# Optimization experiments

Measured on AMD Instinct MI355X. Metric: run time of the kernel, lower is better.

## Reference

```python
import jax, jax.numpy as jnp
import numpy as np


def _bce_logits(x, t):
    # numerically stable BCEWithLogits (pos_weight=1), elementwise
    return jnp.maximum(x, 0.0) - x * t + jnp.log1p(jnp.exp(-jnp.abs(x)))


def _ciou(box1, box2, eps=1e-9):
    # box1, box2: [n,4] in (cx, cy, w, h); matches bbox_iou(..., x1y1x2y2=False, CIoU=True)
    b1x1, b1x2 = box1[:, 0] - box1[:, 2] / 2, box1[:, 0] + box1[:, 2] / 2
    b1y1, b1y2 = box1[:, 1] - box1[:, 3] / 2, box1[:, 1] + box1[:, 3] / 2
    b2x1, b2x2 = box2[:, 0] - box2[:, 2] / 2, box2[:, 0] + box2[:, 2] / 2
    b2y1, b2y2 = box2[:, 1] - box2[:, 3] / 2, box2[:, 1] + box2[:, 3] / 2
    inter = (jnp.clip(jnp.minimum(b1x2, b2x2) - jnp.maximum(b1x1, b2x1), 0.0)
             * jnp.clip(jnp.minimum(b1y2, b2y2) - jnp.maximum(b1y1, b2y1), 0.0))
    w1, h1 = b1x2 - b1x1, b1y2 - b1y1 + eps
    w2, h2 = b2x2 - b2x1, b2y2 - b2y1 + eps
    union = w1 * h1 + w2 * h2 - inter + eps
    iou = inter / union
    cw = jnp.maximum(b1x2, b2x2) - jnp.minimum(b1x1, b2x1)
    ch = jnp.maximum(b1y2, b2y2) - jnp.minimum(b1y1, b2y1)
    c2 = cw ** 2 + ch ** 2 + eps
    rho2 = ((b2x1 + b2x2 - b1x1 - b1x2) ** 2 + (b2y1 + b2y2 - b1y1 - b1y2) ** 2) / 4.0
    v = (4.0 / jnp.pi ** 2) * (jnp.arctan(w2 / h2) - jnp.arctan(w1 / h1)) ** 2
    alpha = jax.lax.stop_gradient(v / (1.0 + eps - iou + v))  # torch.no_grad()
    return iou - (rho2 / c2 + v * alpha)


def _layer_loss(preds, targets, anchors, li):
    # preds: [B, na, H, W, 5+nc]; targets: [nt,6]; anchors: [n_layers, na, 2]
    B, na, H, W, C = preds.shape
    nt = targets.shape[0]
    ai = jnp.arange(na, dtype=preds.dtype)
    # targets.repeat(na,1,1) with anchor index appended -> [na, nt, 7]
    t7 = jnp.concatenate([jnp.broadcast_to(targets[None], (na, nt, 6)),
                          jnp.broadcast_to(ai[:, None, None], (na, nt, 1))], axis=2)
    gain = jnp.array([1.0, 1.0, W, H, W, H, 1.0], dtype=preds.dtype)
    t = t7 * gain
    # anchor-ratio filter: max(r, 1/r).max(-1) < 4 (as boolean mask instead of fancy-index)
    r = t[:, :, 4:6] / anchors[li][:, None, :]                  # [na, nt, 2]
    mask = jnp.max(jnp.maximum(r, 1.0 / r), axis=2) < 4.0       # [na, nt]
    tf = t.reshape(na * nt, 7)
    m = mask.reshape(-1)
    mf = m.astype(preds.dtype)
    b = tf[:, 0].astype(jnp.int32)
    c = tf[:, 1].astype(jnp.int32)
    gxy = tf[:, 2:4]
    gwh = tf[:, 4:6]
    gij = gxy.astype(jnp.int32)  # .long() truncation (coords >= 0)
    gi = jnp.clip(gij[:, 0], 0, W - 1)
    gj = jnp.clip(gij[:, 1], 0, H - 1)
    a = tf[:, 6].astype(jnp.int32)
    # faithful to original: anch = anchors[a] then forward takes [range(n), a] => anchors[a, a]
    anch = anchors[a, a]
    # img_ids = unique(batch ids).flip(); with full 0..B-1 coverage lookup == B-1-b
    match = (B - 1) - b
    ps = preds[match, a, gj, gi]                                # [na*nt, C] gather
    pxy = jax.nn.sigmoid(ps[:, :2])
    pwh = jnp.exp(ps[:, 2:4]) * anch
    pbox = jnp.concatenate([pxy, pwh], axis=1)
    tbox = jnp.concatenate([gxy - gij.astype(gxy.dtype), gwh], axis=1)
    iou = _ciou(pbox, tbox)
    nvalid = jnp.maximum(mf.sum(), 1.0)
    lbox = ((1.0 - iou) * mf).sum() / nvalid                    # mean over matched targets
    # scatter detached clamped iou into tobj; invalid rows get OOB batch idx -> dropped
    scatter_b = jnp.where(m, match, B)
    tobj = jnp.zeros((B, na, H, W), preds.dtype).at[scatter_b, a, gj, gi].set(
        jax.lax.stop_gradient(jnp.clip(iou, 0.0)) * mf)
    nc = C - 5
    t1h = jax.nn.one_hot(c, nc, dtype=preds.dtype)
    lcls = (_bce_logits(ps[:, 5:], t1h) * mf[:, None]).sum() / (nvalid * nc)
    lobj = _bce_logits(preds[..., 4], tobj).mean()
    return lbox, lobj, lcls


def setup_inputs() -> dict:
    key = jax.random.key(0)
    ks = jax.random.split(key, 6)
    p0 = jax.random.normal(ks[0], (16, 3, 80, 80, 85), jnp.float32)
    p1 = jax.random.normal(ks[1], (16, 3, 40, 40, 85), jnp.float32)
    p2 = jax.random.normal(ks[2], (16, 3, 20, 20, 85), jnp.float32)
    nt, B = 300, 16
    img = (jnp.arange(nt) % B).astype(jnp.float32)  # every batch id present
    cls = jax.random.randint(ks[3], (nt,), 0, 80).astype(jnp.float32)
    xy = jax.random.uniform(ks[4], (nt, 2), minval=0.05, maxval=0.95)
    wh = jax.random.uniform(ks[5], (nt, 2), minval=0.02, maxval=0.2)
    targets = jnp.concatenate([img[:, None], cls[:, None], xy, wh], axis=1)
    anchors = jnp.array([[[1.25, 1.625], [2.0, 3.75], [4.125, 2.875]],
                         [[1.875, 3.8125], [3.875, 2.8125], [3.6875, 7.4375]],
                         [[3.625, 2.8125], [4.875, 6.1875], [11.65625, 10.1875]]],
                        dtype=jnp.float32)
    return {"p0": p0, "p1": p1, "p2": p2, "targets": targets, "anchors": anchors}


def reference(p0, p1, p2, targets, anchors):
    lb = lo = lc = 0.0
    for li, p in enumerate((p0, p1, p2)):
        a_, b_, c_ = _layer_loss(p, targets, anchors, li)
        lb = lb + a_
        lo = lo + b_
        lc = lc + c_
    lbox = lb * 0.05
    lobj = lo * 1.0
    lcls = lc * 0.5
    loss = lbox + lobj + lcls
    stats = jnp.stack([lbox, lobj, lcls, loss])
    return (jnp.reshape(loss, (1,)), stats)
```

## Files before the change

kernel.cpp:

```cpp
#include <hip/hip_runtime.h>
#include <math.h>

#define NT    300
#define NA    3
#define BATCH 16
#define NCLS  80
#define CCH   85
#define NROWS 2700
#define NBO   394
#define NBT   675
#define NBLK  (NBO + NBT)
#define HASHSZ 4096


__device__ __forceinline__ float softplusf(float x) {
    return fmaxf(x, 0.f) + log1pf(expf(-fabsf(x)));
}

__device__ __forceinline__ double block_reduce(double v, double* red) {
    #pragma unroll
    for (int off = 32; off > 0; off >>= 1) v += __shfl_down(v, off, 64);
    const int wid = threadIdx.x >> 6, lane = threadIdx.x & 63;
    if (lane == 0) red[wid] = v;
    __syncthreads();
    double r = (threadIdx.x < 4) ? red[threadIdx.x] : 0.0;
    r += __shfl_down(r, 2, 64);
    r += __shfl_down(r, 1, 64);
    __syncthreads();
    return r;
}

__global__ __launch_bounds__(256) void main_kernel(
    const float* __restrict__ p0, const float* __restrict__ p1,
    const float* __restrict__ p2,
    const float* __restrict__ targets, const float* __restrict__ anchors,
    char* __restrict__ ws)
{
    __shared__ double red[4];

    double* obj_part = (double*)(ws);
    float*  row_lbox = (float*)(ws + 3200);
    float*  row_lcls = (float*)(ws + 14000);
    float*  row_nval = (float*)(ws + 24800);
    int*    row_key  = (int*)(ws + 35600);
    float*  row_val  = (float*)(ws + 46400);

    if (blockIdx.x < NBO) {
        const int ob = blockIdx.x;
        int li, bb;
        if (ob < 300)      { li = 0; bb = ob; }
        else if (ob < 375) { li = 1; bb = ob - 300; }
        else               { li = 2; bb = ob - 375; }
        const float* p = (li == 0) ? p0 : ((li == 1) ? p1 : p2);
        const int N = (BATCH * NA * 6400) >> (2*li);

        float s = 0.f;
        #pragma unroll
        for (int k = 0; k < 4; ++k) {
            const int idx = bb * 1024 + k * 256 + threadIdx.x;
            if (idx < N) s += softplusf(p[(size_t)idx * CCH + 4]);
        }
        const double t = block_reduce((double)s, red);
        if (threadIdx.x == 0) obj_part[ob] = t;
        return;
    }

    const int gr   = (blockIdx.x - NBO) * 4 + (threadIdx.x >> 6);
    const int lane = threadIdx.x & 63;
    const int li   = gr / (NA * NT);
    const int r    = gr - li * (NA * NT);
    const int a    = r / NT;
    const int ti   = r - a * NT;
    const float* p = (li == 0) ? p0 : ((li == 1) ? p1 : p2);
    const int W = 80 >> li, H = W;

    const float img = targets[ti*6 + 0];
    const float cls = targets[ti*6 + 1];
    const float tx  = targets[ti*6 + 2] * (float)W;
    const float ty  = targets[ti*6 + 3] * (float)H;
    const float tw  = targets[ti*6 + 4] * (float)W;
    const float th  = targets[ti*6 + 5] * (float)H;

    const float ax = anchors[(li*3 + a)*2 + 0];
    const float ay = anchors[(li*3 + a)*2 + 1];
    const float rx = tw / ax, ry = th / ay;
    const float mr = fmaxf(fmaxf(rx, 1.f/rx), fmaxf(ry, 1.f/ry));
    const bool  mask = mr < 4.f;
    const float mf = mask ? 1.f : 0.f;

    const int b = (int)img;
    const int c = (int)cls;
    const int gij_x = (int)tx;
    const int gij_y = (int)ty;
    const int gi = min(max(gij_x, 0), W - 1);
    const int gj = min(max(gij_y, 0), H - 1);

    const float anch_x = anchors[(a*3 + a)*2 + 0];
    const float anch_y = anchors[(a*3 + a)*2 + 1];

    const int match = BATCH - 1 - b;
    const int cell  = ((match*NA + a)*H + gj)*W + gi;
    const float* ps = p + (size_t)cell * CCH;

    const float x1 = ps[lane];
    const float x2 = (lane < CCH - 64) ? ps[64 + lane] : 0.f;

    const float s0   = __shfl(x1, 0);
    const float s1   = __shfl(x1, 1);
    const float s2   = __shfl(x1, 2);
    const float s3   = __shfl(x1, 3);
    const float objx = __shfl(x1, 4);

    const int ch = 5 + c;
    float contrib = (lane >= 5) ? softplusf(x1) : 0.f;
    if (lane < CCH - 64) contrib += softplusf(x2);
    if (lane == ch) contrib -= x1;
    if (ch >= 64 && lane == ch - 64) contrib -= x2;
    #pragma unroll
    for (int off = 32; off > 0; off >>= 1)
        contrib += __shfl_down(contrib, off, 64);

    const float pxx = 1.f / (1.f + expf(-s0));
    const float pyy = 1.f / (1.f + expf(-s1));
    const float pw  = expf(s2) * anch_x;
    const float ph  = expf(s3) * anch_y;
    const float fx  = tx - (float)gij_x;
    const float fy  = ty - (float)gij_y;

    const float eps = 1e-9f;
    const float b1x1 = pxx - pw*0.5f, b1x2 = pxx + pw*0.5f;
    const float b1y1 = pyy - ph*0.5f, b1y2 = pyy + ph*0.5f;
    const float b2x1 = fx - tw*0.5f,  b2x2 = fx + tw*0.5f;
    const float b2y1 = fy - th*0.5f,  b2y2 = fy + th*0.5f;
    float iw = fminf(b1x2, b2x2) - fmaxf(b1x1, b2x1); iw = fmaxf(iw, 0.f);
    float ih = fminf(b1y2, b2y2) - fmaxf(b1y1, b2y1); ih = fmaxf(ih, 0.f);
    const float inter = iw * ih;
    const float w1 = b1x2 - b1x1, h1 = b1y2 - b1y1 + eps;
    const float w2 = b2x2 - b2x1, h2 = b2y2 - b2y1 + eps;
    const float uni = w1*h1 + w2*h2 - inter + eps;
    const float iou = inter / uni;
    const float cw  = fmaxf(b1x2, b2x2) - fminf(b1x1, b2x1);
    const float chh = fmaxf(b1y2, b2y2) - fminf(b1y1, b2y1);
    const float c2 = cw*cw + chh*chh + eps;
    const float dx = b2x1 + b2x2 - b1x1 - b1x2;
    const float dy = b2y1 + b2y2 - b1y1 - b1y2;
    const float rho2 = (dx*dx + dy*dy) * 0.25f;
    const float dat = atanf(w2/h2) - atanf(w1/h1);
    const float v = 0.40528473456935108577f * dat * dat;
    const float alpha = v / (1.f + eps - iou + v);
    const float ciou = iou - (rho2/c2 + v*alpha);

    if (lane == 0) {
        row_lbox[gr] = (1.f - ciou) * mf;
        row_lcls[gr] = contrib * mf;
        row_nval[gr] = mf;
        row_key[gr]  = mask ? ((li << 20) | cell) : -1;
        row_val[gr]  = mask ? objx * fmaxf(ciou, 0.f) : 0.f;
    }
}

__global__ __launch_bounds__(256) void final_kernel(
    const char* __restrict__ ws, float* __restrict__ out)
{
    __shared__ double red[4];
    __shared__ int hkey[HASHSZ];
    __shared__ int hrow[HASHSZ];

    const double* obj_part = (const double*)(ws);
    const float*  row_lbox = (const float*)(ws + 3200);
    const float*  row_lcls = (const float*)(ws + 14000);
    const float*  row_nval = (const float*)(ws + 24800);
    const int*    row_key  = (const int*)(ws + 35600);
    const float*  row_val  = (const float*)(ws + 46400);

    for (int q = threadIdx.x; q < HASHSZ; q += 256) { hkey[q] = -1; hrow[q] = -1; }
    __syncthreads();

    double so[3] = {0, 0, 0};
    for (int bk = threadIdx.x; bk < NBO; bk += 256) {
        const double v = obj_part[bk];
        if (bk < 300)      so[0] += v;
        else if (bk < 375) so[1] += v;
        else               so[2] += v;
    }

    int    slots[11];
    int    nm = 0;
    double lb[3] = {0,0,0}, lc[3] = {0,0,0}, nv[3] = {0,0,0}, co[3] = {0,0,0};

    for (int i = threadIdx.x; i < NROWS; i += 256) {
        const int l = i / (NA * NT);
        lb[l] += (double)row_lbox[i];
        lc[l] += (double)row_lcls[i];
        nv[l] += (double)row_nval[i];
        const int k = row_key[i];
        int s = -1;
        if (k >= 0) {
            unsigned h = ((unsigned)k * 2654435761u) >> 20;
            s = (int)(h & (HASHSZ - 1));
            while (true) {
                const int prev = atomicCAS(&hkey[s], -1, k);
                if (prev == -1 || prev == k) { atomicMax(&hrow[s], i); break; }
                s = (s + 1) & (HASHSZ - 1);
            }
        }
        slots[nm++] = s;
    }
    __syncthreads();
    nm = 0;
    for (int i = threadIdx.x; i < NROWS; i += 256) {
        const int s = slots[nm++];
        if (s >= 0 && hrow[s] == i)
            co[i / (NA * NT)] += (double)row_val[i];
    }

    double rsum[12];
    #pragma unroll
    for (int l = 0; l < 3; ++l) {
        rsum[l*4 + 0] = block_reduce(lb[l], red);
        rsum[l*4 + 1] = block_reduce(lc[l], red);
        rsum[l*4 + 2] = block_reduce(co[l], red);
        rsum[l*4 + 3] = block_reduce(nv[l], red);
        so[l]         = block_reduce(so[l], red);
    }

    if (threadIdx.x == 0) {
        double lbox = 0.0, lobj = 0.0, lcls = 0.0;
        for (int l = 0; l < 3; ++l) {
            const double nvv = fmax(rsum[l*4 + 3], 1.0);
            lbox += rsum[l*4 + 0] / nvv;
            lcls += rsum[l*4 + 1] / (nvv * (double)NCLS);
            const double N = (double)((BATCH * NA * 6400) >> (2*l));
            lobj += (so[l] - rsum[l*4 + 2]) / N;
        }
        lbox *= 0.05;
        lcls *= 0.5;
        const double loss = lbox + lobj + lcls;
        out[0] = (float)loss;
        out[1] = (float)lbox;
        out[2] = (float)lobj;
        out[3] = (float)lcls;
        out[4] = (float)loss;
    }
}

extern "C" void kernel_launch(void* const* d_in, const int* in_sizes, int n_in,
                              void* d_out, int out_size, void* d_ws, size_t ws_size,
                              hipStream_t stream) {
    const float* p0      = (const float*)d_in[0];
    const float* p1      = (const float*)d_in[1];
    const float* p2      = (const float*)d_in[2];
    const float* targets = (const float*)d_in[3];
    const float* anchors = (const float*)d_in[4];

    main_kernel<<<NBLK, 256, 0, stream>>>(p0, p1, p2, targets, anchors,
                                          (char*)d_ws);
    final_kernel<<<1, 256, 0, stream>>>((const char*)d_ws, (float*)d_out);
}
```

Measured before the change: 183.0 us.

## Resolve duplicate-cell winners in main kernel and pre-reduce per-block partials

Each target row now works out whether a later target with the same image, grid cell and passing anchor filter overrides it, using a wave-wide scan of the targets. This replaces the shared-memory hash table with atomicCAS and atomicMax in the final kernel. The main kernel also sums its four rows per block in shared memory and writes one partial per block, so the final kernel only does small reductions. The cost is an extra O(NT) scan per row in the main kernel, while the serialized single-block hashing goes away.

```diff
diff --git a/kernel.cpp b/kernel.cpp
--- a/kernel.cpp
+++ b/kernel.cpp
@@ -6,11 +6,9 @@
 #define BATCH 16
 #define NCLS  80
 #define CCH   85
-#define NROWS 2700
 #define NBO   394
 #define NBT   675
 #define NBLK  (NBO + NBT)
-#define HASHSZ 4096
 
 
 __device__ __forceinline__ float softplusf(float x) {
@@ -37,13 +35,10 @@
     char* __restrict__ ws)
 {
     __shared__ double red[4];
-
-    double* obj_part = (double*)(ws);
-    float*  row_lbox = (float*)(ws + 3200);
-    float*  row_lcls = (float*)(ws + 14000);
-    float*  row_nval = (float*)(ws + 24800);
-    int*    row_key  = (int*)(ws + 35600);
-    float*  row_val  = (float*)(ws + 46400);
+    __shared__ double acc[4][4];
+
+    double* obj_part = (double*)ws;
+    double* tgt_part = (double*)(ws + 3200);
 
     if (blockIdx.x < NBO) {
         const int ob = blockIdx.x;
@@ -65,7 +60,8 @@
         return;
     }
 
-    const int gr   = (blockIdx.x - NBO) * 4 + (threadIdx.x >> 6);
+    const int tb   = blockIdx.x - NBO;
+    const int gr   = tb * 4 + (threadIdx.x >> 6);
     const int lane = threadIdx.x & 63;
     const int li   = gr / (NA * NT);
     const int r    = gr - li * (NA * NT);
@@ -94,6 +90,23 @@
     const int gij_y = (int)ty;
     const int gi = min(max(gij_x, 0), W - 1);
     const int gj = min(max(gij_y, 0), H - 1);
+
+    bool beaten = false;
+    for (int tj = ti + 1 + lane; tj < NT; tj += 64) {
+        const float img_j = targets[tj*6 + 0];
+        const float xj = targets[tj*6 + 2] * (float)W;
+        const float yj = targets[tj*6 + 3] * (float)H;
+        const float wj = targets[tj*6 + 4] * (float)W;
+        const float hj = targets[tj*6 + 5] * (float)H;
+        const float rxj = wj / ax, ryj = hj / ay;
+        const float mrj = fmaxf(fmaxf(rxj, 1.f/rxj), fmaxf(ryj, 1.f/ryj));
+        if (mrj < 4.f && img_j == img) {
+            const int gi_j = min(max((int)xj, 0), W - 1);
+            const int gj_j = min(max((int)yj, 0), H - 1);
+            if (gi_j == gi && gj_j == gj) beaten = true;
+        }
+    }
+    const bool winner = mask && !__any(beaten);
 
     const float anch_x = anchors[(a*3 + a)*2 + 0];
     const float anch_y = anchors[(a*3 + a)*2 + 1];
@@ -151,11 +164,17 @@
     const float ciou = iou - (rho2/c2 + v*alpha);
 
     if (lane == 0) {
-        row_lbox[gr] = (1.f - ciou) * mf;
-        row_lcls[gr] = contrib * mf;
-        row_nval[gr] = mf;
-        row_key[gr]  = mask ? ((li << 20) | cell) : -1;
-        row_val[gr]  = mask ? objx * fmaxf(ciou, 0.f) : 0.f;
+        const int wid = threadIdx.x >> 6;
+        acc[wid][0] = (double)((1.f - ciou) * mf);
+        acc[wid][1] = (double)(contrib * mf);
+        acc[wid][2] = (double)mf;
+        acc[wid][3] = winner ? (double)(objx * fmaxf(ciou, 0.f)) : 0.0;
+    }
+    __syncthreads();
+    if (threadIdx.x < 4) {
+        tgt_part[tb*4 + threadIdx.x] =
+            acc[0][threadIdx.x] + acc[1][threadIdx.x] +
+            acc[2][threadIdx.x] + acc[3][threadIdx.x];
     }
 }
 
@@ -163,75 +182,42 @@
     const char* __restrict__ ws, float* __restrict__ out)
 {
     __shared__ double red[4];
-    __shared__ int hkey[HASHSZ];
-    __shared__ int hrow[HASHSZ];
-
-    const double* obj_part = (const double*)(ws);
-    const float*  row_lbox = (const float*)(ws + 3200);
-    const float*  row_lcls = (const float*)(ws + 14000);
-    const float*  row_nval = (const float*)(ws + 24800);
-    const int*    row_key  = (const int*)(ws + 35600);
-    const float*  row_val  = (const float*)(ws + 46400);
-
-    for (int q = threadIdx.x; q < HASHSZ; q += 256) { hkey[q] = -1; hrow[q] = -1; }
-    __syncthreads();
-
-    double so[3] = {0, 0, 0};
+    const double* obj_part = (const double*)ws;
+    const double* tgt_part = (const double*)(ws + 3200);
+
+    double so[3] = {0,0,0};
+    double lb[3] = {0,0,0}, lc[3] = {0,0,0}, nv[3] = {0,0,0}, co[3] = {0,0,0};
+
     for (int bk = threadIdx.x; bk < NBO; bk += 256) {
-        const double v = obj_part[bk];
-        if (bk < 300)      so[0] += v;
-        else if (bk < 375) so[1] += v;
-        else               so[2] += v;
-    }
-
-    int    slots[11];
-    int    nm = 0;
-    double lb[3] = {0,0,0}, lc[3] = {0,0,0}, nv[3] = {0,0,0}, co[3] = {0,0,0};
-
-    for (int i = threadIdx.x; i < NROWS; i += 256) {
-        const int l = i / (NA * NT);
-        lb[l] += (double)row_lbox[i];
-        lc[l] += (double)row_lcls[i];
-        nv[l] += (double)row_nval[i];
-        const int k = row_key[i];
-        int s = -1;
-        if (k >= 0) {
-            unsigned h = ((unsigned)k * 2654435761u) >> 20;
-            s = (int)(h & (HASHSZ - 1));
-            while (true) {
-                const int prev = atomicCAS(&hkey[s], -1, k);
-                if (prev == -1 || prev == k) { atomicMax(&hrow[s], i); break; }
-                s = (s + 1) & (HASHSZ - 1);
-            }
-        }
-        slots[nm++] = s;
-    }
-    __syncthreads();
-    nm = 0;
-    for (int i = threadIdx.x; i < NROWS; i += 256) {
-        const int s = slots[nm++];
-        if (s >= 0 && hrow[s] == i)
-            co[i / (NA * NT)] += (double)row_val[i];
-    }
-
-    double rsum[12];
+        const int l = (bk < 300) ? 0 : ((bk < 375) ? 1 : 2);
+        so[l] += obj_part[bk];
+    }
+    for (int tb = threadIdx.x; tb < NBT; tb += 256) {
+        const int l = (tb < 225) ? 0 : ((tb < 450) ? 1 : 2);
+        lb[l] += tgt_part[tb*4 + 0];
+        lc[l] += tgt_part[tb*4 + 1];
+        nv[l] += tgt_part[tb*4 + 2];
+        co[l] += tgt_part[tb*4 + 3];
+    }
+
+    double rsum[15];
     #pragma unroll
     for (int l = 0; l < 3; ++l) {
-        rsum[l*4 + 0] = block_reduce(lb[l], red);
-        rsum[l*4 + 1] = block_reduce(lc[l], red);
-        rsum[l*4 + 2] = block_reduce(co[l], red);
-        rsum[l*4 + 3] = block_reduce(nv[l], red);
-        so[l]         = block_reduce(so[l], red);
+        rsum[l*5 + 0] = block_reduce(lb[l], red);
+        rsum[l*5 + 1] = block_reduce(lc[l], red);
+        rsum[l*5 + 2] = block_reduce(co[l], red);
+        rsum[l*5 + 3] = block_reduce(nv[l], red);
+        rsum[l*5 + 4] = block_reduce(so[l], red);
     }
 
     if (threadIdx.x == 0) {
         double lbox = 0.0, lobj = 0.0, lcls = 0.0;
         for (int l = 0; l < 3; ++l) {
-            const double nvv = fmax(rsum[l*4 + 3], 1.0);
-            lbox += rsum[l*4 + 0] / nvv;
-            lcls += rsum[l*4 + 1] / (nvv * (double)NCLS);
+            const double nvv = fmax(rsum[l*5 + 3], 1.0);
+            lbox += rsum[l*5 + 0] / nvv;
+            lcls += rsum[l*5 + 1] / (nvv * (double)NCLS);
             const double N = (double)((BATCH * NA * 6400) >> (2*l));
-            lobj += (so[l] - rsum[l*4 + 2]) / N;
+            lobj += (rsum[l*5 + 4] - rsum[l*5 + 2]) / N;
         }
         lbox *= 0.05;
         lcls *= 0.5;
```

Result: faster. 178.0 us (-2.7%).
